# Kernel tuning notes

Hardware: AMD Instinct MI355X
Metric: run time of the kernel (lower is better)

The kernel has to match this reference:

```python
import jax, jax.numpy as jnp
import numpy as np

B, C, H, V = 16384, 5, 256, 512
NUM_ITER = 2


def setup_inputs() -> dict:
    key = jax.random.key(0)
    k1, k2, k3, k4 = jax.random.split(key, 4)
    # v0: one-hot categorical visible units, shape [B, C, V, 1]
    idx = jax.random.randint(k1, (B, V), 0, C)
    v0 = jax.nn.one_hot(idx, C, axis=1, dtype=jnp.float32)[..., None]
    W = 0.01 * jax.random.normal(k2, (C, H, V), dtype=jnp.float32)
    b = 0.01 * jax.random.normal(k3, (C, V, 1), dtype=jnp.float32)
    c = 0.01 * jax.random.normal(k4, (H, 1), dtype=jnp.float32)
    return {"v0": v0, "W": W, "b": b, "c": c, "num_sampling_iter": NUM_ITER}


def reference(v0, W, b, c, num_sampling_iter):
    key = jax.random.key(42)
    b2 = b[..., 0]   # [C, V]
    c1 = c[:, 0]     # [H]
    v = v0[..., 0]   # [B, C, V]

    def sample_h(k, v):
        # p(h=1|v) = sigmoid(sum_c W[c] @ v[:,c] + c)
        p = jax.nn.sigmoid(jnp.einsum('chv,bcv->bh', W, v) + c1)  # [B, H]
        return jax.random.bernoulli(k, p).astype(v.dtype)

    def sample_v(k, h):
        # logits over categories per visible unit: W[c].T @ h + b[c]
        logits = jnp.einsum('chv,bh->bcv', W, h) + b2  # [B, C, V]
        idx = jax.random.categorical(k, logits, axis=1)  # [B, V]
        return jax.nn.one_hot(idx, C, axis=1, dtype=h.dtype)  # [B, C, V]

    keys = jax.random.split(key, 2 * num_sampling_iter + 1)
    h = sample_h(keys[0], v)
    h_given_v0 = h
    for i in range(num_sampling_iter):  # small fixed iteration count
        v = sample_v(keys[2 * i + 1], h)
        h = sample_h(keys[2 * i + 2], v)
    return (v[..., None], h[..., None], h_given_v0[..., None])
```

## Files before the change

kernel.cpp:

```cpp
#include <hip/hip_runtime.h>
#include <cstdint>
#include <cstddef>


#define B_DIM 16384
#define C_DIM 5
#define H_DIM 256
#define V_DIM 512
#define KC    320

struct TFOut { uint32_t a, b; };

typedef float f32x2 __attribute__((ext_vector_type(2)));
typedef float f32x4 __attribute__((ext_vector_type(4)));

static __device__ inline f32x2 mk2(float x, float y) {
  f32x2 r; r.x = x; r.y = y; return r;
}

static __device__ inline f32x2 pkfma(f32x2 a, f32x2 b, f32x2 c) {
#if __has_builtin(__builtin_elementwise_fma)
  return __builtin_elementwise_fma(a, b, c);
#else
  f32x2 r; r.x = fmaf(a.x, b.x, c.x); r.y = fmaf(a.y, b.y, c.y); return r;
#endif
}

__host__ __device__ static inline TFOut tf2x32(uint32_t k0, uint32_t k1,
                                               uint32_t c0, uint32_t c1) {
  uint32_t ks2 = k0 ^ k1 ^ 0x1BD11BDAu;
  uint32_t x0 = c0 + k0, x1 = c1 + k1;
#define TF_R(r) { x0 += x1; x1 = (x1 << r) | (x1 >> (32 - r)); x1 ^= x0; }
  TF_R(13) TF_R(15) TF_R(26) TF_R(6)
  x0 += k1;  x1 += ks2 + 1u;
  TF_R(17) TF_R(29) TF_R(16) TF_R(24)
  x0 += ks2; x1 += k0 + 2u;
  TF_R(13) TF_R(15) TF_R(26) TF_R(6)
  x0 += k0;  x1 += k1 + 3u;
  TF_R(17) TF_R(29) TF_R(16) TF_R(24)
  x0 += k1;  x1 += ks2 + 4u;
  TF_R(13) TF_R(15) TF_R(26) TF_R(6)
  x0 += ks2; x1 += k0 + 5u;
#undef TF_R
  TFOut o; o.a = x0; o.b = x1; return o;
}

__device__ static inline uint32_t rng_bits(uint32_t k0, uint32_t k1, uint32_t i) {
  TFOut r = tf2x32(k0, k1, 0u, i);
  return r.a ^ r.b;
}

__device__ static inline float bits_to_unit_float(uint32_t bits) {
  return __uint_as_float((bits >> 9) | 0x3F800000u) - 1.0f;
}

__device__ static float xla_exp(float x_in) {
#pragma clang fp contract(off)
  float x = fminf(x_in, 88.3762626647950f);
  x = fmaxf(x, -88.3762626647949f);
  float fx = floorf(x * 1.44269504088896341f + 0.5f);
  float tmp = fx * 0.693359375f;
  float z = fx * -2.12194440e-4f;
  x = x - tmp;
  x = x - z;
  z = x * x;
  float y = 1.9875691500e-4f;
  y = y * x + 1.3981999507e-3f;
  y = y * x + 8.3334519073e-3f;
  y = y * x + 4.1665795894e-2f;
  y = y * x + 1.6666665459e-1f;
  y = y * x + 5.0000001201e-1f;
  y = y * z + x;
  y = y + 1.0f;
  int n = (int)fx;
  y = y * __uint_as_float((uint32_t)(n + 127) << 23);
  return y;
}

__device__ static float xla_log(float x_in) {
#pragma clang fp contract(off)
  float xv = fmaxf(x_in, 1.17549435e-38f);
  uint32_t bits = __float_as_uint(xv);
  float e = (float)((int)(bits >> 23) - 126);
  float x = __uint_as_float((bits & 0x007FFFFFu) | 0x3F000000u);
  bool m = (x < 0.707106781186547524f);
  float tmp = m ? x : 0.0f;
  x = x - 1.0f;
  e = e - (m ? 1.0f : 0.0f);
  x = x + tmp;
  float z = x * x;
  float y = 7.0376836292e-2f;
  y = y * x + -1.1514610310e-1f;
  y = y * x + 1.1676998740e-1f;
  y = y * x + -1.2420140846e-1f;
  y = y * x + 1.4249322787e-1f;
  y = y * x + -1.6668057665e-1f;
  y = y * x + 2.0000714765e-1f;
  y = y * x + -2.4999993993e-1f;
  y = y * x + 3.3333331174e-1f;
  y = y * x;
  y = y * z;
  float t1 = e * -2.12194440e-4f;
  y = y + t1;
  float t2 = z * 0.5f;
  y = y - t2;
  x = x + y;
  float t3 = e * 0.693359375f;
  x = x + t3;
  return x;
}


__global__ void k_sentinel(float* out, float d) {
  out[0] = d;
}

__global__ __launch_bounds__(256) void k_idx(const float* __restrict__ v0,
                                             uint8_t* __restrict__ idx) {
  int t = blockIdx.x * 256 + threadIdx.x;
  int b = t >> 9, v = t & 511;
  const float* p = v0 + (size_t)b * (C_DIM * V_DIM) + v;
  int cf = 0;
#pragma unroll
  for (int c = 0; c < C_DIM; ++c)
    if (p[c * V_DIM] > 0.5f) cf = c;
  idx[t] = (uint8_t)cf;
}

__global__ __launch_bounds__(256) void k_wt(const float* __restrict__ W,
                                            float* __restrict__ Wt) {
  int t = blockIdx.x * 256 + threadIdx.x;
  int h = t & 255; int rest = t >> 8; int v = rest & 511; int c = rest >> 9;
  Wt[t] = W[((size_t)c * H_DIM + h) * V_DIM + v];
}

__global__ __launch_bounds__(256) void k_sample_h(
    const float* __restrict__ Wt, const float* __restrict__ c1,
    const uint8_t* __restrict__ idx,
    float* __restrict__ out_h, uint32_t* __restrict__ out_mask,
    uint32_t key0, uint32_t key1) {
  __shared__ uint8_t  sidx[V_DIM];
  __shared__ uint32_t soff[V_DIM];
  __shared__ uint16_t cnt[8][5];
  __shared__ uint16_t base[8][5];
  __shared__ uint16_t jb[10];
  int b = blockIdx.x;
  int t = threadIdx.x;
  if (t < 128)
    ((uint32_t*)sidx)[t] = ((const uint32_t*)(idx + (size_t)b * V_DIM))[t];
  __syncthreads();

  int lane = t & 63, wv = t >> 6;
  int v0 = t,       c0 = sidx[v0];
  int v1 = t + 256, c1i = sidx[v1];
  int rank0, rank1;
  {
    unsigned long long bal[5];
#pragma unroll
    for (int cc = 0; cc < 5; ++cc) bal[cc] = __ballot(c0 == cc);
    if (lane == 0) {
#pragma unroll
      for (int cc = 0; cc < 5; ++cc) cnt[wv][cc] = (uint16_t)__popcll(bal[cc]);
    }
    rank0 = (int)__popcll(bal[c0] & ((1ull << lane) - 1ull));
  }
  {
    unsigned long long bal[5];
#pragma unroll
    for (int cc = 0; cc < 5; ++cc) bal[cc] = __ballot(c1i == cc);
    if (lane == 0) {
#pragma unroll
      for (int cc = 0; cc < 5; ++cc) cnt[4 + wv][cc] = (uint16_t)__popcll(bal[cc]);
    }
    rank1 = (int)__popcll(bal[c1i] & ((1ull << lane) - 1ull));
  }
  __syncthreads();
  if (t == 0) {
    int pos = 0;
    for (int cc = 0; cc < 5; ++cc)
      for (int g = 0; g < 8; ++g) { base[g][cc] = (uint16_t)pos; pos += cnt[g][cc]; }
  }
  __syncthreads();
  soff[base[wv][c0] + rank0]       = (uint32_t)(c0 * V_DIM + v0) << 10;
  soff[base[4 + wv][c1i] + rank1]  = (uint32_t)(c1i * V_DIM + v1) << 10;
  __syncthreads();
  if (t < 10) {
    uint32_t target = (uint32_t)(t * KC) << 10;
    int lo = 0, hi = V_DIM;
    while (lo < hi) { int mid = (lo + hi) >> 1;
      if (soff[mid] < target) lo = mid + 1; else hi = mid; }
    jb[t] = (uint16_t)lo;
  }
  __syncthreads();

  const char* Wh = (const char*)Wt + (size_t)t * 4;
  float total = 0.0f;
  for (int s = 0; s < 9; ++s) {
    int j = jb[s], jend = jb[s + 1];
    float psum = 0.0f;
    for (; j + 4 <= jend; j += 4) {
      float w0 = *(const float*)(Wh + soff[j]);
      float w1 = *(const float*)(Wh + soff[j + 1]);
      float w2 = *(const float*)(Wh + soff[j + 2]);
      float w3 = *(const float*)(Wh + soff[j + 3]);
      psum += w0; psum += w1; psum += w2; psum += w3;
    }
    for (; j < jend; ++j) psum += *(const float*)(Wh + soff[j]);
    total += psum;
  }

  float tt = total + c1[t];
  float p = 1.0f / (1.0f + xla_exp(-tt));

  uint32_t i = (uint32_t)(b * H_DIM + t);
  float u = bits_to_unit_float(rng_bits(key0, key1, i));
  bool hb = (u < p);
  if (out_h) out_h[(size_t)b * H_DIM + t] = hb ? 1.0f : 0.0f;

  unsigned long long m = __ballot(hb);
  if ((t & 63) == 0) {
    out_mask[(size_t)b * 8 + wv * 2 + 0] = (uint32_t)(m & 0xFFFFFFFFull);
    out_mask[(size_t)b * 8 + wv * 2 + 1] = (uint32_t)(m >> 32);
  }
}

static __device__ inline void gv_h(float2 w2, const float* tbf_row,
                                   f32x2* av0, f32x2* av1) {
  f32x2 ww0 = mk2(w2.x, w2.x);
  f32x2 ww1 = mk2(w2.y, w2.y);
  const f32x4* fp = (const f32x4*)tbf_row;
  f32x4 qA = fp[0], qB = fp[1], qC = fp[2], qD = fp[3];
  f32x2 f0 = __builtin_shufflevector(qA, qA, 0, 1);
  f32x2 f1 = __builtin_shufflevector(qA, qA, 2, 3);
  f32x2 f2 = __builtin_shufflevector(qB, qB, 0, 1);
  f32x2 f3 = __builtin_shufflevector(qB, qB, 2, 3);
  f32x2 f4 = __builtin_shufflevector(qC, qC, 0, 1);
  f32x2 f5 = __builtin_shufflevector(qC, qC, 2, 3);
  f32x2 f6 = __builtin_shufflevector(qD, qD, 0, 1);
  f32x2 f7 = __builtin_shufflevector(qD, qD, 2, 3);
  av0[0] = pkfma(ww0, f0, av0[0]); av1[0] = pkfma(ww1, f0, av1[0]);
  av0[1] = pkfma(ww0, f1, av0[1]); av1[1] = pkfma(ww1, f1, av1[1]);
  av0[2] = pkfma(ww0, f2, av0[2]); av1[2] = pkfma(ww1, f2, av1[2]);
  av0[3] = pkfma(ww0, f3, av0[3]); av1[3] = pkfma(ww1, f3, av1[3]);
  av0[4] = pkfma(ww0, f4, av0[4]); av1[4] = pkfma(ww1, f4, av1[4]);
  av0[5] = pkfma(ww0, f5, av0[5]); av1[5] = pkfma(ww1, f5, av1[5]);
  av0[6] = pkfma(ww0, f6, av0[6]); av1[6] = pkfma(ww1, f6, av1[6]);
  av0[7] = pkfma(ww0, f7, av0[7]); av1[7] = pkfma(ww1, f7, av1[7]);
}

__global__ __launch_bounds__(256, 4) void k_gemm_v(
    const float* __restrict__ W, const uint32_t* __restrict__ mask,
    float* __restrict__ sums) {
  __shared__ uint32_t smask[16][8];
  __shared__ __align__(16) float tbf[H_DIM][16];
  int t = threadIdx.x;
  int b0 = blockIdx.x * 16;
  if (t < 128) smask[t >> 3][t & 7] = mask[(size_t)b0 * 8 + t];
  __syncthreads();
  {
    int h = t;
    uint32_t w = (uint32_t)(h >> 5), s = (uint32_t)(h & 31), x = 0;
#pragma unroll
    for (int j = 0; j < 16; ++j)
      x |= ((smask[j][w] >> s) & 1u) << j;
#pragma unroll
    for (int i = 0; i < 16; ++i)
      tbf[h][i] = (float)((x >> i) & 1u);
  }
  __syncthreads();

  int wv = t >> 6, lane = t & 63;
  int v0 = wv * 128 + (lane << 1);

  for (int c = 0; c < C_DIM; ++c) {
    f32x2 av0[8], av1[8];
#pragma unroll
    for (int j = 0; j < 8; ++j) {
      av0[j] = mk2(0.f, 0.f);
      av1[j] = mk2(0.f, 0.f);
    }
    const float* wp = W + (size_t)c * (H_DIM * V_DIM) + v0;
    for (int hh = 0; hh < H_DIM; hh += 8) {
      float2 w8[8];
#pragma unroll
      for (int u = 0; u < 8; ++u)
        w8[u] = *(const float2*)(wp + (size_t)(hh + u) * V_DIM);
#pragma unroll
      for (int u = 0; u < 8; ++u)
        gv_h(w8[u], &tbf[hh + u][0], av0, av1);
    }
#pragma unroll
    for (int j = 0; j < 8; ++j) {
      float2 oA; oA.x = av0[j].x; oA.y = av1[j].x;
      *(float2*)&sums[((size_t)c * B_DIM + b0 + 2 * j) * V_DIM + v0] = oA;
      float2 oB; oB.x = av0[j].y; oB.y = av1[j].y;
      *(float2*)&sums[((size_t)c * B_DIM + b0 + 2 * j + 1) * V_DIM + v0] = oB;
    }
  }
}

__global__ __launch_bounds__(256, 4) void k_gumbel_v(
    const float* __restrict__ sums, const float* __restrict__ b2,
    uint8_t* __restrict__ idx_out, uint32_t key0, uint32_t key1) {
  int gidx = blockIdx.x * 256 + threadIdx.x;
  int b = gidx >> 7;
  int v0 = (gidx & 127) << 2;
  float best[4];
  uint32_t bc = 0;
#pragma unroll
  for (int c = 0; c < C_DIM; ++c) {
    float4 av = *(const float4*)&sums[((size_t)c * B_DIM + b) * V_DIM + v0];
    float4 bv = *(const float4*)&b2[c * V_DIM + v0];
    uint32_t ib = ((uint32_t)b * C_DIM + (uint32_t)c) * V_DIM + (uint32_t)v0;
    float avq[4] = {av.x, av.y, av.z, av.w};
    float bvq[4] = {bv.x, bv.y, bv.z, bv.w};
#pragma unroll
    for (int q = 0; q < 4; ++q) {
      float uf = bits_to_unit_float(rng_bits(key0, key1, ib + (uint32_t)q));
      if (uf == 0.0f) uf = 1.17549435e-38f;
      float gz = -xla_log(-xla_log(uf));
      float z = gz + (avq[q] + bvq[q]);
      if (c == 0 || z > best[q]) {
        best[q] = z;
        bc = (bc & ~(0xFFu << (8 * q))) | ((uint32_t)c << (8 * q));
      }
    }
  }
  *(uint32_t*)(idx_out + (size_t)b * V_DIM + v0) = bc;
}

__global__ __launch_bounds__(256) void k_onehot(const uint8_t* __restrict__ idx,
                                                float* __restrict__ out) {
  int t = blockIdx.x * 256 + threadIdx.x;
  int v = t & 511; int rest = t >> 9; int c = rest % C_DIM; int b = rest / C_DIM;
  out[t] = (idx[(size_t)b * V_DIM + v] == c) ? 1.0f : 0.0f;
}


extern "C" void kernel_launch(void* const* d_in, const int* in_sizes, int n_in,
                              void* d_out, int out_size, void* d_ws, size_t ws_size,
                              hipStream_t stream) {
  float* out = (float*)d_out;

  const size_t WS_NEED = 2621440ull
                       + 2621440ull
                       + 8388608ull
                       + 524288ull;
  float D = 0.0f;
  if (n_in < 4)                       D = 910.0f + (float)n_in;
  else if (in_sizes[0] != 41943040)   D = 920.0f;
  else if (in_sizes[1] != 655360)     D = 921.0f;
  else if (in_sizes[2] != 2560)       D = 922.0f;
  else if (in_sizes[3] != 256)        D = 923.0f;
  else if (out_size != 50331648)      D = 930.0f + (float)out_size * 1e-6f;
  else if (ws_size < WS_NEED)         D = 100.0f + (float)(ws_size >> 20);
  if (D != 0.0f) {
    hipLaunchKernelGGL(k_sentinel, dim3(1), dim3(1), 0, stream, out, D);
    return;
  }

  const float* v0 = (const float*)d_in[0];
  const float* W  = (const float*)d_in[1];
  const float* b2 = (const float*)d_in[2];
  const float* c1 = (const float*)d_in[3];

  float* out_v  = out;
  float* out_h  = out + (size_t)B_DIM * C_DIM * V_DIM;
  float* out_h0 = out_h + (size_t)B_DIM * H_DIM;

  char* ws = (char*)d_ws;
  float*    Wt   = (float*)(ws);
  uint8_t*  idx  = (uint8_t*)(ws + 5242880);
  uint32_t* mask = (uint32_t*)(ws + 13631488);

  float* sums = out_v;

  uint32_t keys[5][2];
  for (int i = 0; i < 5; ++i) {
    TFOut r = tf2x32(0u, 42u, 0u, (uint32_t)i);
    keys[i][0] = r.a; keys[i][1] = r.b;
  }

  hipLaunchKernelGGL(k_wt,  dim3(2560),  dim3(256), 0, stream, W, Wt);
  hipLaunchKernelGGL(k_idx, dim3(32768), dim3(256), 0, stream, v0, idx);

  hipLaunchKernelGGL(k_sample_h, dim3(B_DIM), dim3(256), 0, stream,
                     Wt, c1, idx, out_h0, mask, keys[0][0], keys[0][1]);
  hipLaunchKernelGGL(k_gemm_v, dim3(B_DIM / 16), dim3(256), 0, stream,
                     W, mask, sums);
  hipLaunchKernelGGL(k_gumbel_v, dim3(B_DIM * 128 / 256), dim3(256), 0, stream,
                     sums, b2, idx, keys[1][0], keys[1][1]);
  hipLaunchKernelGGL(k_sample_h, dim3(B_DIM), dim3(256), 0, stream,
                     Wt, c1, idx, (float*)nullptr, mask, keys[2][0], keys[2][1]);
  hipLaunchKernelGGL(k_gemm_v, dim3(B_DIM / 16), dim3(256), 0, stream,
                     W, mask, sums);
  hipLaunchKernelGGL(k_gumbel_v, dim3(B_DIM * 128 / 256), dim3(256), 0, stream,
                     sums, b2, idx, keys[3][0], keys[3][1]);
  hipLaunchKernelGGL(k_sample_h, dim3(B_DIM), dim3(256), 0, stream,
                     Wt, c1, idx, out_h, mask, keys[4][0], keys[4][1]);
  hipLaunchKernelGGL(k_onehot, dim3(163840), dim3(256), 0, stream, idx, out_v);
}
```

Before: 2.033 ms.

## Enlarge gemm_v register tile to 16 batch by 4 visibles per thread

Restructures the visible-logits GEMM so each block handles 32 batch rows and each thread accumulates a 16x4 tile (float4 W loads) instead of 16x2. Two wave groups split the batch rows and two split the visible dimension, which halves the number of blocks and raises arithmetic intensity per W load and per shared-memory read. The transposed hidden-bit buffer doubles to 32 columns and launch bounds drop to 2 blocks per SM because more accumulator registers are needed, which lowers occupancy.

```diff
diff --git a/kernel.cpp b/kernel.cpp
--- a/kernel.cpp
+++ b/kernel.cpp
@@ -224,77 +224,83 @@
   }
 }
 
-static __device__ inline void gv_h(float2 w2, const float* tbf_row,
-                                   f32x2* av0, f32x2* av1) {
-  f32x2 ww0 = mk2(w2.x, w2.x);
-  f32x2 ww1 = mk2(w2.y, w2.y);
-  const f32x4* fp = (const f32x4*)tbf_row;
-  f32x4 qA = fp[0], qB = fp[1], qC = fp[2], qD = fp[3];
-  f32x2 f0 = __builtin_shufflevector(qA, qA, 0, 1);
-  f32x2 f1 = __builtin_shufflevector(qA, qA, 2, 3);
-  f32x2 f2 = __builtin_shufflevector(qB, qB, 0, 1);
-  f32x2 f3 = __builtin_shufflevector(qB, qB, 2, 3);
-  f32x2 f4 = __builtin_shufflevector(qC, qC, 0, 1);
-  f32x2 f5 = __builtin_shufflevector(qC, qC, 2, 3);
-  f32x2 f6 = __builtin_shufflevector(qD, qD, 0, 1);
-  f32x2 f7 = __builtin_shufflevector(qD, qD, 2, 3);
-  av0[0] = pkfma(ww0, f0, av0[0]); av1[0] = pkfma(ww1, f0, av1[0]);
-  av0[1] = pkfma(ww0, f1, av0[1]); av1[1] = pkfma(ww1, f1, av1[1]);
-  av0[2] = pkfma(ww0, f2, av0[2]); av1[2] = pkfma(ww1, f2, av1[2]);
-  av0[3] = pkfma(ww0, f3, av0[3]); av1[3] = pkfma(ww1, f3, av1[3]);
-  av0[4] = pkfma(ww0, f4, av0[4]); av1[4] = pkfma(ww1, f4, av1[4]);
-  av0[5] = pkfma(ww0, f5, av0[5]); av1[5] = pkfma(ww1, f5, av1[5]);
-  av0[6] = pkfma(ww0, f6, av0[6]); av1[6] = pkfma(ww1, f6, av1[6]);
-  av0[7] = pkfma(ww0, f7, av0[7]); av1[7] = pkfma(ww1, f7, av1[7]);
-}
-
-__global__ __launch_bounds__(256, 4) void k_gemm_v(
+__global__ __launch_bounds__(256, 2) void k_gemm_v(
     const float* __restrict__ W, const uint32_t* __restrict__ mask,
     float* __restrict__ sums) {
-  __shared__ uint32_t smask[16][8];
-  __shared__ __align__(16) float tbf[H_DIM][16];
+  __shared__ uint32_t smask[32][8];
+  __shared__ __align__(16) float tbf[H_DIM][32];
   int t = threadIdx.x;
-  int b0 = blockIdx.x * 16;
-  if (t < 128) smask[t >> 3][t & 7] = mask[(size_t)b0 * 8 + t];
+  int b0 = blockIdx.x * 32;
+  smask[t >> 3][t & 7] = mask[(size_t)b0 * 8 + t];
   __syncthreads();
   {
     int h = t;
-    uint32_t w = (uint32_t)(h >> 5), s = (uint32_t)(h & 31), x = 0;
-#pragma unroll
-    for (int j = 0; j < 16; ++j)
-      x |= ((smask[j][w] >> s) & 1u) << j;
-#pragma unroll
-    for (int i = 0; i < 16; ++i)
-      tbf[h][i] = (float)((x >> i) & 1u);
+    uint32_t w = (uint32_t)(h >> 5), s = (uint32_t)(h & 31);
+#pragma unroll
+    for (int j = 0; j < 32; ++j)
+      tbf[h][j] = (float)((smask[j][w] >> s) & 1u);
   }
   __syncthreads();
 
   int wv = t >> 6, lane = t & 63;
-  int v0 = wv * 128 + (lane << 1);
+  int g = wv >> 1, vh = wv & 1;
+  int v0 = vh * 256 + (lane << 2);
+  int bg = b0 + g * 16;
 
   for (int c = 0; c < C_DIM; ++c) {
-    f32x2 av0[8], av1[8];
-#pragma unroll
-    for (int j = 0; j < 8; ++j) {
-      av0[j] = mk2(0.f, 0.f);
-      av1[j] = mk2(0.f, 0.f);
-    }
+    f32x2 acc[8][4];
+#pragma unroll
+    for (int p = 0; p < 8; ++p)
+#pragma unroll
+      for (int q = 0; q < 4; ++q) acc[p][q] = mk2(0.f, 0.f);
+
     const float* wp = W + (size_t)c * (H_DIM * V_DIM) + v0;
-    for (int hh = 0; hh < H_DIM; hh += 8) {
-      float2 w8[8];
-#pragma unroll
-      for (int u = 0; u < 8; ++u)
-        w8[u] = *(const float2*)(wp + (size_t)(hh + u) * V_DIM);
-#pragma unroll
-      for (int u = 0; u < 8; ++u)
-        gv_h(w8[u], &tbf[hh + u][0], av0, av1);
-    }
-#pragma unroll
-    for (int j = 0; j < 8; ++j) {
-      float2 oA; oA.x = av0[j].x; oA.y = av1[j].x;
-      *(float2*)&sums[((size_t)c * B_DIM + b0 + 2 * j) * V_DIM + v0] = oA;
-      float2 oB; oB.x = av0[j].y; oB.y = av1[j].y;
-      *(float2*)&sums[((size_t)c * B_DIM + b0 + 2 * j + 1) * V_DIM + v0] = oB;
+    for (int hh = 0; hh < H_DIM; hh += 4) {
+      float4 w4[4];
+#pragma unroll
+      for (int u = 0; u < 4; ++u)
+        w4[u] = *(const float4*)(wp + (size_t)(hh + u) * V_DIM);
+#pragma unroll
+      for (int u = 0; u < 4; ++u) {
+        const f32x4* fp = (const f32x4*)&tbf[hh + u][g * 16];
+        f32x4 qA = fp[0], qB = fp[1], qC = fp[2], qD = fp[3];
+        f32x2 f0 = __builtin_shufflevector(qA, qA, 0, 1);
+        f32x2 f1 = __builtin_shufflevector(qA, qA, 2, 3);
+        f32x2 f2 = __builtin_shufflevector(qB, qB, 0, 1);
+        f32x2 f3 = __builtin_shufflevector(qB, qB, 2, 3);
+        f32x2 f4 = __builtin_shufflevector(qC, qC, 0, 1);
+        f32x2 f5 = __builtin_shufflevector(qC, qC, 2, 3);
+        f32x2 f6 = __builtin_shufflevector(qD, qD, 0, 1);
+        f32x2 f7 = __builtin_shufflevector(qD, qD, 2, 3);
+        f32x2 wwx = mk2(w4[u].x, w4[u].x);
+        f32x2 wwy = mk2(w4[u].y, w4[u].y);
+        f32x2 wwz = mk2(w4[u].z, w4[u].z);
+        f32x2 www = mk2(w4[u].w, w4[u].w);
+        acc[0][0] = pkfma(wwx, f0, acc[0][0]); acc[0][1] = pkfma(wwy, f0, acc[0][1]);
+        acc[0][2] = pkfma(wwz, f0, acc[0][2]); acc[0][3] = pkfma(www, f0, acc[0][3]);
+        acc[1][0] = pkfma(wwx, f1, acc[1][0]); acc[1][1] = pkfma(wwy, f1, acc[1][1]);
+        acc[1][2] = pkfma(wwz, f1, acc[1][2]); acc[1][3] = pkfma(www, f1, acc[1][3]);
+        acc[2][0] = pkfma(wwx, f2, acc[2][0]); acc[2][1] = pkfma(wwy, f2, acc[2][1]);
+        acc[2][2] = pkfma(wwz, f2, acc[2][2]); acc[2][3] = pkfma(www, f2, acc[2][3]);
+        acc[3][0] = pkfma(wwx, f3, acc[3][0]); acc[3][1] = pkfma(wwy, f3, acc[3][1]);
+        acc[3][2] = pkfma(wwz, f3, acc[3][2]); acc[3][3] = pkfma(www, f3, acc[3][3]);
+        acc[4][0] = pkfma(wwx, f4, acc[4][0]); acc[4][1] = pkfma(wwy, f4, acc[4][1]);
+        acc[4][2] = pkfma(wwz, f4, acc[4][2]); acc[4][3] = pkfma(www, f4, acc[4][3]);
+        acc[5][0] = pkfma(wwx, f5, acc[5][0]); acc[5][1] = pkfma(wwy, f5, acc[5][1]);
+        acc[5][2] = pkfma(wwz, f5, acc[5][2]); acc[5][3] = pkfma(www, f5, acc[5][3]);
+        acc[6][0] = pkfma(wwx, f6, acc[6][0]); acc[6][1] = pkfma(wwy, f6, acc[6][1]);
+        acc[6][2] = pkfma(wwz, f6, acc[6][2]); acc[6][3] = pkfma(www, f6, acc[6][3]);
+        acc[7][0] = pkfma(wwx, f7, acc[7][0]); acc[7][1] = pkfma(wwy, f7, acc[7][1]);
+        acc[7][2] = pkfma(wwz, f7, acc[7][2]); acc[7][3] = pkfma(www, f7, acc[7][3]);
+      }
+    }
+#pragma unroll
+    for (int p = 0; p < 8; ++p) {
+      float4 oA, oB;
+      oA.x = acc[p][0].x; oA.y = acc[p][1].x; oA.z = acc[p][2].x; oA.w = acc[p][3].x;
+      oB.x = acc[p][0].y; oB.y = acc[p][1].y; oB.z = acc[p][2].y; oB.w = acc[p][3].y;
+      *(float4*)&sums[((size_t)c * B_DIM + bg + 2 * p) * V_DIM + v0] = oA;
+      *(float4*)&sums[((size_t)c * B_DIM + bg + 2 * p + 1) * V_DIM + v0] = oB;
     }
   }
 }
@@ -386,13 +392,13 @@
 
   hipLaunchKernelGGL(k_sample_h, dim3(B_DIM), dim3(256), 0, stream,
                      Wt, c1, idx, out_h0, mask, keys[0][0], keys[0][1]);
-  hipLaunchKernelGGL(k_gemm_v, dim3(B_DIM / 16), dim3(256), 0, stream,
+  hipLaunchKernelGGL(k_gemm_v, dim3(B_DIM / 32), dim3(256), 0, stream,
                      W, mask, sums);
   hipLaunchKernelGGL(k_gumbel_v, dim3(B_DIM * 128 / 256), dim3(256), 0, stream,
                      sums, b2, idx, keys[1][0], keys[1][1]);
   hipLaunchKernelGGL(k_sample_h, dim3(B_DIM), dim3(256), 0, stream,
                      Wt, c1, idx, (float*)nullptr, mask, keys[2][0], keys[2][1]);
-  hipLaunchKernelGGL(k_gemm_v, dim3(B_DIM / 16), dim3(256), 0, stream,
+  hipLaunchKernelGGL(k_gemm_v, dim3(B_DIM / 32), dim3(256), 0, stream,
                      W, mask, sums);
   hipLaunchKernelGGL(k_gumbel_v, dim3(B_DIM * 128 / 256), dim3(256), 0, stream,
                      sums, b2, idx, keys[3][0], keys[3][1]);
```

Result: faster. 1.980 ms (-2.6%).
